# Performance work log

Measured on AMD Instinct MI355X. Metric: run time of the kernel, lower is better.

The kernel has to match this reference:

```python
import jax, jax.numpy as jnp
import numpy as np

N_NODES = 100000
N_EDGES = 1600000
HIDDEN = 128
STEPS = 4
N_GRAPHS = 64


def setup_inputs() -> dict:
    key = jax.random.key(0)
    ks = jax.random.split(key, 8)
    x = jax.random.normal(ks[0], (N_NODES, HIDDEN), dtype=jnp.float32)
    edge_index = jax.random.randint(ks[1], (2, N_EDGES), 0, N_NODES, dtype=jnp.int64)
    batch = jnp.sort(jax.random.randint(ks[2], (N_NODES,), 0, N_GRAPHS, dtype=jnp.int64))
    s = 1.0 / np.sqrt(HIDDEN)
    weight = jax.random.normal(ks[3], (STEPS, HIDDEN, HIDDEN), dtype=jnp.float32) * s
    w_ih = jax.random.normal(ks[4], (3 * HIDDEN, HIDDEN), dtype=jnp.float32) * s
    w_hh = jax.random.normal(ks[5], (3 * HIDDEN, HIDDEN), dtype=jnp.float32) * s
    b_ih = jnp.zeros((3 * HIDDEN,), dtype=jnp.float32)
    b_hh = jnp.zeros((3 * HIDDEN,), dtype=jnp.float32)
    return {"x": x, "edge_index": edge_index, "batch": batch,
            "weight": weight, "w_ih": w_ih, "w_hh": w_hh,
            "b_ih": b_ih, "b_hh": b_hh}


def _gru_cell(m, h, w_ih, w_hh, b_ih, b_hh):
    # PyTorch GRUCell: gates ordered (r, z, n)
    gi = m @ w_ih.T + b_ih  # [N, 3H]
    gh = h @ w_hh.T + b_hh  # [N, 3H]
    i_r, i_z, i_n = jnp.split(gi, 3, axis=-1)
    h_r, h_z, h_n = jnp.split(gh, 3, axis=-1)
    r = jax.nn.sigmoid(i_r + h_r)
    z = jax.nn.sigmoid(i_z + h_z)
    n = jnp.tanh(i_n + r * h_n)
    return (1.0 - z) * n + z * h


def reference(x, edge_index, batch, weight, w_ih, w_hh, b_ih, b_hh):
    src, dst = edge_index[0], edge_index[1]
    h = x
    for i in range(STEPS):
        m = h @ weight[i]  # [N, H]
        # message = m[src] scattered (add) into dst
        aggr = jax.ops.segment_sum(m[src], dst, num_segments=N_NODES)
        h = _gru_cell(aggr, h, w_ih, w_hh, b_ih, b_hh)
    h = jax.nn.relu(h)
    # global mean pool per graph
    sums = jax.ops.segment_sum(h, batch, num_segments=N_GRAPHS)  # [G, H]
    counts = jax.ops.segment_sum(jnp.ones((N_NODES,), h.dtype), batch, num_segments=N_GRAPHS)
    return sums / jnp.maximum(counts, 1.0)[:, None]
```

## Files before the change

### kernel.cpp

```cpp
#include <hip/hip_runtime.h>

#define N_NODES  100000
#define N_EDGES  1600000
#define HIDDEN   128
#define STEPS    4
#define N_GRAPHS 64
#define NBUCK    256
#define BWID     391
#define BCAP     7168

typedef unsigned short u16;
typedef unsigned int   u32;
typedef unsigned long long u64;
typedef __attribute__((ext_vector_type(8))) short bf16x8;
typedef __attribute__((ext_vector_type(4))) float f32x4;
typedef __attribute__((ext_vector_type(2))) float f32x2;

__device__ inline u16 f2bf(float f) {
  u32 u = __float_as_uint(f);
  u = (u + 0x7FFFu + ((u >> 16) & 1u)) >> 16;
  return (u16)u;
}
__device__ inline float bf2f(u16 b) { return __uint_as_float(((u32)b) << 16); }

__device__ inline float rcp_f(float x) { return __builtin_amdgcn_rcpf(x); }
__device__ inline float sig_f(float x) { return rcp_f(1.f + __expf(-x)); }
__device__ inline float tanh_f(float x) { return 1.f - 2.f * rcp_f(1.f + __expf(2.f * x)); }

__global__ __launch_bounds__(1024) void k_part(const int* __restrict__ esrc,
                                               const int* __restrict__ edst,
                                               int* __restrict__ gcursor,
                                               u32* __restrict__ ebuf) {
  __shared__ int hist[16][NBUCK];
  __shared__ int base[16][NBUCK];
  int tid = threadIdx.x;
  int wv  = tid >> 6;
  #pragma unroll
  for (int i = 0; i < 4; ++i) ((int*)hist)[tid + i * 1024] = 0;
  __syncthreads();
  int e0 = blockIdx.x * 4096;
  int sv[4], dv[4], bk[4], rk[4];
  #pragma unroll
  for (int i = 0; i < 4; ++i) {
    int e = e0 + i * 1024 + tid;
    if (e < N_EDGES) {
      sv[i] = esrc[e];
      dv[i] = edst[e];
      bk[i] = (int)((u32)dv[i] / (u32)BWID);
      rk[i] = atomicAdd(&hist[wv][bk[i]], 1);
    } else bk[i] = -1;
  }
  __syncthreads();
  if (tid < NBUCK) {
    int c[16];
    int sum = 0;
    #pragma unroll
    for (int w = 0; w < 16; ++w) { c[w] = hist[w][tid]; sum += c[w]; }
    int g = atomicAdd(&gcursor[tid], sum);
    #pragma unroll
    for (int w = 0; w < 16; ++w) { base[w][tid] = g; g += c[w]; }
  }
  __syncthreads();
  #pragma unroll
  for (int i = 0; i < 4; ++i) {
    if (bk[i] >= 0) {
      int pos = bk[i] * BCAP + base[wv][bk[i]] + rk[i];
      ebuf[pos] = ((u32)(dv[i] - bk[i] * BWID) << 17) | (u32)sv[i];
    }
  }
}

__global__ void k_bscan(const int* __restrict__ gcursor, int* __restrict__ ebase,
                        float* __restrict__ acc) {
  __shared__ int buf[NBUCK];
  int t = threadIdx.x;
  int v = gcursor[t];
  buf[t] = v;
  __syncthreads();
  for (int off = 1; off < NBUCK; off <<= 1) {
    int u = 0;
    if (t >= off) u = buf[t - off];
    __syncthreads();
    buf[t] += u;
    __syncthreads();
  }
  ebase[t] = buf[t] - v;
  if (t == NBUCK - 1) ebase[NBUCK] = buf[t];
  for (int i = t; i < N_GRAPHS * HIDDEN; i += NBUCK) acc[i] = 0.f;
}

__global__ __launch_bounds__(1024) void k_csr(const u32* __restrict__ ebuf,
                                              const int* __restrict__ ebase,
                                              int* __restrict__ offs,
                                              int* __restrict__ csr) {
  __shared__ int lcnt[512];
  __shared__ int lofs[512];
  int b = blockIdx.x, tid = threadIdx.x;
  int n0 = b * BWID;
  int n1 = min(n0 + BWID, N_NODES);
  int nn = n1 - n0;
  int e0 = ebase[b];
  int cnt = ebase[b + 1] - e0;
  const u32* ebase_p = ebuf + (size_t)b * BCAP;
  if (tid < 512) lcnt[tid] = 0;
  __syncthreads();
  for (int e = tid; e < cnt; e += 1024) {
    int dst = (int)(ebase_p[e] >> 17);
    atomicAdd(&lcnt[dst], 1);
  }
  __syncthreads();
  if (tid < 512) lofs[tid] = lcnt[tid];
  __syncthreads();
  for (int off = 1; off < 512; off <<= 1) {
    int v = 0;
    if (tid < 512 && tid >= off) v = lofs[tid - off];
    __syncthreads();
    if (tid < 512 && tid >= off) lofs[tid] += v;
    __syncthreads();
  }
  int nodeoff = 0;
  if (tid < 512) nodeoff = e0 + lofs[tid] - lcnt[tid];
  if (tid < 512) lofs[tid] = nodeoff;
  if (tid < nn) offs[n0 + tid] = nodeoff;
  if (b == 0 && tid == 0) offs[N_NODES] = N_EDGES;
  __syncthreads();
  for (int e = tid; e < cnt; e += 1024) {
    u32 p = ebase_p[e];
    int src = (int)(p & 0x1FFFFu);
    int dst = (int)(p >> 17);
    int pos = atomicAdd(&lofs[dst], 1);
    csr[pos] = src;
  }
}

__global__ void k_wb(const float* __restrict__ W, const float* __restrict__ w_ih,
                     const float* __restrict__ w_hh, u16* __restrict__ bsw) {
  __shared__ float wrow[128];
  int b = blockIdx.x, st = b >> 8, k = b & 255, t = threadIdx.x;
  if (k < 128) wrow[t] = W[(st * 128 + k) * 128 + t];
  __syncthreads();
  int kc = k >> 5, quad = (k >> 3) & 3, kl = k & 7;
  u16* base = bsw + (size_t)st * 131072 + kc * 16384;
  #pragma unroll
  for (int gq = 0; gq < 4; ++gq) {
    int c = gq * 128 + t;
    float v;
    if (k < 128) {
      if (c < 384) {
        const float* wr = w_ih + c * 128;
        float sacc = 0.f;
        for (int j = 0; j < 128; ++j) sacc += wrow[j] * wr[j];
        v = sacc;
      } else v = 0.f;
    } else {
      int kk = k - 128;
      if (c < 256)      v = w_hh[c * 128 + kk];
      else if (c < 384) v = 0.f;
      else              v = w_hh[(c - 128) * 128 + kk];
    }
    int gi = c >> 7, cw = c & 127;
    int wv = cw >> 5, hu = (cw >> 4) & 1, nl = c & 15;
    int slot = wv * 8 + gi * 2 + hu;
    base[(slot * 4 + quad) * 128 + nl * 8 + kl] = f2bf(v);
  }
}

__global__ void k_convert(const float* __restrict__ x, u16* __restrict__ h0,
                          u16* __restrict__ h1) {
  int i = (blockIdx.x * 256 + threadIdx.x) * 4;
  float4 v = *(const float4*)(x + i);
  u16 o[4] = {f2bf(v.x), f2bf(v.y), f2bf(v.z), f2bf(v.w)};
  *(uint2*)(h0 + i) = *(uint2*)o;
  if (blockIdx.x == 0) {
    int t = threadIdx.x;
    if (t < 64)       ((u32*)(h0 + (size_t)N_NODES * 128))[t] = 0;
    else if (t < 128) ((u32*)(h1 + (size_t)N_NODES * 128))[t - 64] = 0;
  }
}

__device__ inline void acc8(f32x2* a, uint4 p) {
  f32x2 v;
  v.x = __uint_as_float(p.x << 16); v.y = __uint_as_float(p.x & 0xffff0000u);
  a[0] += v;
  v.x = __uint_as_float(p.y << 16); v.y = __uint_as_float(p.y & 0xffff0000u);
  a[1] += v;
  v.x = __uint_as_float(p.z << 16); v.y = __uint_as_float(p.z & 0xffff0000u);
  a[2] += v;
  v.x = __uint_as_float(p.w << 16); v.y = __uint_as_float(p.w & 0xffff0000u);
  a[3] += v;
}
__device__ inline uint4 ldrow(const char* hb, u32 off) {
  return *(const uint4*)(hb + off);
}

__global__ void k_gather(const u16* __restrict__ h, const int* __restrict__ csr,
                         const int* __restrict__ offs, u16* __restrict__ s) {
  int node = blockIdx.x * 4 + (threadIdx.x >> 6);
  int lane = threadIdx.x & 63;
  int q   = lane >> 4;
  int sub = lane & 15;
  const char* hb = (const char*)h;
  u32 co = (u32)(sub * 16);
  int beg = offs[node], end = offs[node + 1];
  f32x2 a[4];
  a[0] = a[1] = a[2] = a[3] = (f32x2){0.f, 0.f};
  int j = beg + q;
  for (; j + 12 < end; j += 16) {
    u32 s0 = (u32)csr[j], s1 = (u32)csr[j + 4], s2 = (u32)csr[j + 8], s3 = (u32)csr[j + 12];
    uint4 p0 = ldrow(hb, (s0 << 8) | co);
    uint4 p1 = ldrow(hb, (s1 << 8) | co);
    uint4 p2 = ldrow(hb, (s2 << 8) | co);
    uint4 p3 = ldrow(hb, (s3 << 8) | co);
    acc8(a, p0); acc8(a, p1); acc8(a, p2); acc8(a, p3);
  }
  {
    int j0 = j, j1 = j + 4, j2 = j + 8, j3 = j + 12;
    int t0 = (j0 < end) ? j0 : 0, t1 = (j1 < end) ? j1 : 0;
    int t2 = (j2 < end) ? j2 : 0, t3 = (j3 < end) ? j3 : 0;
    u32 s0 = (u32)csr[t0]; s0 = (j0 < end) ? s0 : (u32)N_NODES;
    u32 s1 = (u32)csr[t1]; s1 = (j1 < end) ? s1 : (u32)N_NODES;
    u32 s2 = (u32)csr[t2]; s2 = (j2 < end) ? s2 : (u32)N_NODES;
    u32 s3 = (u32)csr[t3]; s3 = (j3 < end) ? s3 : (u32)N_NODES;
    uint4 p0 = ldrow(hb, (s0 << 8) | co);
    uint4 p1 = ldrow(hb, (s1 << 8) | co);
    uint4 p2 = ldrow(hb, (s2 << 8) | co);
    uint4 p3 = ldrow(hb, (s3 << 8) | co);
    acc8(a, p0); acc8(a, p1); acc8(a, p2); acc8(a, p3);
  }
  #pragma unroll
  for (int i = 0; i < 4; ++i) {
    a[i].x += __shfl_xor(a[i].x, 16); a[i].x += __shfl_xor(a[i].x, 32);
    a[i].y += __shfl_xor(a[i].y, 16); a[i].y += __shfl_xor(a[i].y, 32);
  }
  if (q == 0) {
    uint4 o;
    o.x = (u32)f2bf(a[0].x) | ((u32)f2bf(a[0].y) << 16);
    o.y = (u32)f2bf(a[1].x) | ((u32)f2bf(a[1].y) << 16);
    o.z = (u32)f2bf(a[2].x) | ((u32)f2bf(a[2].y) << 16);
    o.w = (u32)f2bf(a[3].x) | ((u32)f2bf(a[3].y) << 16);
    *(uint4*)(s + (size_t)node * 128 + sub * 8) = o;
  }
}

__global__ __launch_bounds__(256, 2) void k_gemm_gru(
    const u16* __restrict__ s_mat, const u16* __restrict__ h_mat,
    const u16* __restrict__ bsw, const float* __restrict__ b_ih,
    const float* __restrict__ b_hh, u16* __restrict__ h_out) {
  __shared__ u16 Asw[8192];

  const int tid  = threadIdx.x;
  const int wave = tid >> 6;
  const int lane = tid & 63;
  const int nl   = lane & 15;
  const int quad = lane >> 4;
  const int row0 = blockIdx.x * 32;

  {
    int snl = tid & 15, squad = (tid >> 4) & 3, sel = tid >> 6;
    int g = sel & 1, half = sel >> 1;
    const u16* row = (half ? h_mat : s_mat) + (size_t)(row0 + g * 16 + snl) * 128;
    #pragma unroll
    for (int kc2 = 0; kc2 < 4; ++kc2) {
      uint4 v = *(const uint4*)(row + kc2 * 32 + squad * 8);
      *(uint4*)&Asw[(((g * 8 + half * 4 + kc2) * 4 + squad) * 16 + snl) * 8] = v;
    }
  }
  __syncthreads();

  const u16* bp = bsw + wave * 8 * 512 + lane * 8;

  f32x4 acc[2][8];
  #pragma unroll
  for (int g = 0; g < 2; ++g)
    #pragma unroll
    for (int u = 0; u < 8; ++u) acc[g][u] = (f32x4){0.f, 0.f, 0.f, 0.f};

  bf16x8 b0[6], b1[6], b2[6];
  #pragma unroll
  for (int i = 0; i < 6; ++i) b0[i] = *(const bf16x8*)(bp + i * 512);
  #pragma unroll
  for (int i = 0; i < 6; ++i) b1[i] = *(const bf16x8*)(bp + 16384 + i * 512);

  #pragma unroll
  for (int kc = 0; kc < 8; ++kc) {
    if (kc < 6) {
      #pragma unroll
      for (int i = 0; i < 6; ++i) {
        int us = (kc + 2 < 4) ? i : (i < 4 ? i : i + 2);
        b2[i] = *(const bf16x8*)(bp + (kc + 2) * 16384 + us * 512);
      }
    }
    bf16x8 a0 = *(const bf16x8*)&Asw[kc * 512 + lane * 8];
    bf16x8 a1 = *(const bf16x8*)&Asw[(8 + kc) * 512 + lane * 8];
    #pragma unroll
    for (int i = 0; i < 6; ++i) {
      int u = (kc < 4) ? i : (i < 4 ? i : i + 2);
      acc[0][u] = __builtin_amdgcn_mfma_f32_16x16x32_bf16(a0, b0[i], acc[0][u], 0, 0, 0);
      acc[1][u] = __builtin_amdgcn_mfma_f32_16x16x32_bf16(a1, b0[i], acc[1][u], 0, 0, 0);
    }
    #pragma unroll
    for (int i = 0; i < 6; ++i) { b0[i] = b1[i]; b1[i] = b2[i]; }
  }

  float bias[8];
  #pragma unroll
  for (int u = 0; u < 8; ++u) {
    int gi = u >> 1, hu = u & 1;
    int cw = wave * 32 + hu * 16 + nl;
    bias[u] = (gi == 0) ? b_ih[cw] + b_hh[cw]
            : (gi == 1) ? b_ih[128 + cw] + b_hh[128 + cw]
            : (gi == 2) ? b_ih[256 + cw]
                        : b_hh[256 + cw];
  }

  #pragma unroll
  for (int g = 0; g < 2; ++g) {
    #pragma unroll
    for (int hu = 0; hu < 2; ++hu) {
      int cw = wave * 32 + hu * 16 + nl;
      int hbase = ((g * 8 + 4 + wave) * 4 + ((hu * 2 + (nl >> 3)) & 3)) * 128 + (nl & 7);
      #pragma unroll
      for (int i = 0; i < 4; ++i) {
        int m = quad * 4 + i;
        float rv = sig_f(acc[g][0 + hu][i] + bias[0 + hu]);
        float zv = sig_f(acc[g][2 + hu][i] + bias[2 + hu]);
        float iv = acc[g][4 + hu][i] + bias[4 + hu];
        float hn = acc[g][6 + hu][i] + bias[6 + hu];
        float hv = bf2f(Asw[hbase + m * 8]);
        float n  = tanh_f(iv + rv * hn);
        float o  = n + zv * (hv - n);
        h_out[(size_t)(row0 + g * 16 + m) * 128 + cw] = f2bf(o);
      }
    }
  }
}

__global__ void k_pool_partial(const u16* __restrict__ h, const int* __restrict__ batch,
                               float* __restrict__ acc) {
  int t = threadIdx.x;
  int node0 = blockIdx.x * 125;
  int node1 = node0 + 125;
  int cur = batch[node0];
  float sum = 0.f;
  for (int r = node0; r < node1; ++r) {
    int g = batch[r];
    if (g != cur) {
      atomicAdd(&acc[cur * 128 + t], sum);
      sum = 0.f;
      cur = g;
    }
    sum += fmaxf(bf2f(h[(size_t)r * 128 + t]), 0.f);
  }
  atomicAdd(&acc[cur * 128 + t], sum);
}

__global__ void k_pool_div(const float* __restrict__ acc, const int* __restrict__ batch,
                           float* __restrict__ out) {
  __shared__ int se[2];
  int g = blockIdx.x, t = threadIdx.x;
  if (t < 2) {
    int target = g + t;
    int lo = 0, hi = N_NODES;
    while (lo < hi) { int mid = (lo + hi) >> 1; if (batch[mid] < target) lo = mid + 1; else hi = mid; }
    se[t] = lo;
  }
  __syncthreads();
  int cnt = se[1] - se[0];
  out[g * 128 + t] = acc[g * 128 + t] / (float)(cnt > 0 ? cnt : 1);
}

extern "C" void kernel_launch(void* const* d_in, const int* in_sizes, int n_in,
                              void* d_out, int out_size, void* d_ws, size_t ws_size,
                              hipStream_t stream) {
  const float* x     = (const float*)d_in[0];
  const int*   edges = (const int*)d_in[1];
  const int*   batch = (const int*)d_in[2];
  const float* W     = (const float*)d_in[3];
  const float* w_ih  = (const float*)d_in[4];
  const float* w_hh  = (const float*)d_in[5];
  const float* b_ih  = (const float*)d_in[6];
  const float* b_hh  = (const float*)d_in[7];
  float* out = (float*)d_out;

  char* w = (char*)d_ws;
  u16* buf0    = (u16*)(w);
  u16* buf1    = (u16*)(w + 25600256);
  u16* bsw     = (u16*)(w + 51200512);
  float* acc   = (float*)(w + 52249088);
  int* offs    = (int*)(w + 52281856);
  int* gcursor = (int*)(w + 52682240);
  int* ebase   = (int*)(w + 52683264);
  int* csr     = (int*)(w + 52684800);
  u32* ebuf    = (u32*)buf1;

  const int* esrc = edges;
  const int* edst = edges + N_EDGES;

  hipMemsetAsync(gcursor, 0, NBUCK * sizeof(int), stream);
  k_part<<<391, 1024, 0, stream>>>(esrc, edst, gcursor, ebuf);
  k_bscan<<<1, NBUCK, 0, stream>>>(gcursor, ebase, acc);
  k_csr<<<NBUCK, 1024, 0, stream>>>(ebuf, ebase, offs, csr);
  k_wb<<<1024, 128, 0, stream>>>(W, w_ih, w_hh, bsw);
  k_convert<<<(N_NODES * HIDDEN) / 1024, 256, 0, stream>>>(x, buf0, buf1);

  u16* hcur = buf0;
  u16* hnxt = buf1;
  for (int st = 0; st < STEPS; ++st) {
    k_gather<<<N_NODES / 4, 256, 0, stream>>>(hcur, csr, offs, hnxt);
    k_gemm_gru<<<N_NODES / 32, 256, 0, stream>>>(hnxt, hcur, bsw + st * 131072,
                                                 b_ih, b_hh, hnxt);
    u16* tmp = hcur; hcur = hnxt; hnxt = tmp;
  }
  k_pool_partial<<<800, 128, 0, stream>>>(hcur, batch, acc);
  k_pool_div<<<N_GRAPHS, 128, 0, stream>>>(acc, batch, out);
}
```

Baseline: 585.5 us.

## Fuse neighbor gather into GEMM+GRU kernel, staging aggregates in shared memory

Merges the per-step CSR gather kernel into the GEMM+GRU kernel. Each wave gathers 8 nodes' neighbor sums and writes them as bf16 directly into the swizzled shared-memory A tile, while the h half is still loaded from global. This removes the global write and re-read of the aggregated matrix and one launch per step. The cost is that the latency-bound gather now runs at the GEMM's low occupancy (launch bounds of 256 threads, 2 blocks), with each wave walking its 8 nodes in sequence, so load latency may be poorly hidden.

New measurement: 616.7 us. 1.05x slower.

```diff
diff --git a/kernel.cpp b/kernel.cpp
--- a/kernel.cpp
+++ b/kernel.cpp
@@ -193,59 +193,11 @@
   return *(const uint4*)(hb + off);
 }
 
-__global__ void k_gather(const u16* __restrict__ h, const int* __restrict__ csr,
-                         const int* __restrict__ offs, u16* __restrict__ s) {
-  int node = blockIdx.x * 4 + (threadIdx.x >> 6);
-  int lane = threadIdx.x & 63;
-  int q   = lane >> 4;
-  int sub = lane & 15;
-  const char* hb = (const char*)h;
-  u32 co = (u32)(sub * 16);
-  int beg = offs[node], end = offs[node + 1];
-  f32x2 a[4];
-  a[0] = a[1] = a[2] = a[3] = (f32x2){0.f, 0.f};
-  int j = beg + q;
-  for (; j + 12 < end; j += 16) {
-    u32 s0 = (u32)csr[j], s1 = (u32)csr[j + 4], s2 = (u32)csr[j + 8], s3 = (u32)csr[j + 12];
-    uint4 p0 = ldrow(hb, (s0 << 8) | co);
-    uint4 p1 = ldrow(hb, (s1 << 8) | co);
-    uint4 p2 = ldrow(hb, (s2 << 8) | co);
-    uint4 p3 = ldrow(hb, (s3 << 8) | co);
-    acc8(a, p0); acc8(a, p1); acc8(a, p2); acc8(a, p3);
-  }
-  {
-    int j0 = j, j1 = j + 4, j2 = j + 8, j3 = j + 12;
-    int t0 = (j0 < end) ? j0 : 0, t1 = (j1 < end) ? j1 : 0;
-    int t2 = (j2 < end) ? j2 : 0, t3 = (j3 < end) ? j3 : 0;
-    u32 s0 = (u32)csr[t0]; s0 = (j0 < end) ? s0 : (u32)N_NODES;
-    u32 s1 = (u32)csr[t1]; s1 = (j1 < end) ? s1 : (u32)N_NODES;
-    u32 s2 = (u32)csr[t2]; s2 = (j2 < end) ? s2 : (u32)N_NODES;
-    u32 s3 = (u32)csr[t3]; s3 = (j3 < end) ? s3 : (u32)N_NODES;
-    uint4 p0 = ldrow(hb, (s0 << 8) | co);
-    uint4 p1 = ldrow(hb, (s1 << 8) | co);
-    uint4 p2 = ldrow(hb, (s2 << 8) | co);
-    uint4 p3 = ldrow(hb, (s3 << 8) | co);
-    acc8(a, p0); acc8(a, p1); acc8(a, p2); acc8(a, p3);
-  }
-  #pragma unroll
-  for (int i = 0; i < 4; ++i) {
-    a[i].x += __shfl_xor(a[i].x, 16); a[i].x += __shfl_xor(a[i].x, 32);
-    a[i].y += __shfl_xor(a[i].y, 16); a[i].y += __shfl_xor(a[i].y, 32);
-  }
-  if (q == 0) {
-    uint4 o;
-    o.x = (u32)f2bf(a[0].x) | ((u32)f2bf(a[0].y) << 16);
-    o.y = (u32)f2bf(a[1].x) | ((u32)f2bf(a[1].y) << 16);
-    o.z = (u32)f2bf(a[2].x) | ((u32)f2bf(a[2].y) << 16);
-    o.w = (u32)f2bf(a[3].x) | ((u32)f2bf(a[3].y) << 16);
-    *(uint4*)(s + (size_t)node * 128 + sub * 8) = o;
-  }
-}
-
-__global__ __launch_bounds__(256, 2) void k_gemm_gru(
-    const u16* __restrict__ s_mat, const u16* __restrict__ h_mat,
-    const u16* __restrict__ bsw, const float* __restrict__ b_ih,
-    const float* __restrict__ b_hh, u16* __restrict__ h_out) {
+__global__ __launch_bounds__(256, 2) void k_fused(
+    const u16* __restrict__ h_mat, const int* __restrict__ csr,
+    const int* __restrict__ offs, const u16* __restrict__ bsw,
+    const float* __restrict__ b_ih, const float* __restrict__ b_hh,
+    u16* __restrict__ h_out) {
   __shared__ u16 Asw[8192];
 
   const int tid  = threadIdx.x;
@@ -257,12 +209,66 @@
 
   {
     int snl = tid & 15, squad = (tid >> 4) & 3, sel = tid >> 6;
-    int g = sel & 1, half = sel >> 1;
-    const u16* row = (half ? h_mat : s_mat) + (size_t)(row0 + g * 16 + snl) * 128;
-    #pragma unroll
-    for (int kc2 = 0; kc2 < 4; ++kc2) {
-      uint4 v = *(const uint4*)(row + kc2 * 32 + squad * 8);
-      *(uint4*)&Asw[(((g * 8 + half * 4 + kc2) * 4 + squad) * 16 + snl) * 8] = v;
+    if (sel >= 2) {
+      int g = sel & 1;
+      const u16* row = h_mat + (size_t)(row0 + g * 16 + snl) * 128;
+      #pragma unroll
+      for (int kc2 = 0; kc2 < 4; ++kc2) {
+        uint4 v = *(const uint4*)(row + kc2 * 32 + squad * 8);
+        *(uint4*)&Asw[(((g * 8 + 4 + kc2) * 4 + squad) * 16 + snl) * 8] = v;
+      }
+    }
+  }
+
+  {
+    const char* hb = (const char*)h_mat;
+    const int q   = lane >> 4;
+    const int sub = lane & 15;
+    const u32 co  = (u32)(sub * 16);
+    #pragma unroll 1
+    for (int i = 0; i < 8; ++i) {
+      int n    = wave * 8 + i;
+      int node = row0 + n;
+      int beg = offs[node], end = offs[node + 1];
+      f32x2 a[4];
+      a[0] = a[1] = a[2] = a[3] = (f32x2){0.f, 0.f};
+      int j = beg + q;
+      for (; j + 12 < end; j += 16) {
+        u32 s0 = (u32)csr[j], s1 = (u32)csr[j + 4], s2 = (u32)csr[j + 8], s3 = (u32)csr[j + 12];
+        uint4 p0 = ldrow(hb, (s0 << 8) | co);
+        uint4 p1 = ldrow(hb, (s1 << 8) | co);
+        uint4 p2 = ldrow(hb, (s2 << 8) | co);
+        uint4 p3 = ldrow(hb, (s3 << 8) | co);
+        acc8(a, p0); acc8(a, p1); acc8(a, p2); acc8(a, p3);
+      }
+      {
+        int j0 = j, j1 = j + 4, j2 = j + 8, j3 = j + 12;
+        int t0 = (j0 < end) ? j0 : 0, t1 = (j1 < end) ? j1 : 0;
+        int t2 = (j2 < end) ? j2 : 0, t3 = (j3 < end) ? j3 : 0;
+        u32 s0 = (u32)csr[t0]; s0 = (j0 < end) ? s0 : (u32)N_NODES;
+        u32 s1 = (u32)csr[t1]; s1 = (j1 < end) ? s1 : (u32)N_NODES;
+        u32 s2 = (u32)csr[t2]; s2 = (j2 < end) ? s2 : (u32)N_NODES;
+        u32 s3 = (u32)csr[t3]; s3 = (j3 < end) ? s3 : (u32)N_NODES;
+        uint4 p0 = ldrow(hb, (s0 << 8) | co);
+        uint4 p1 = ldrow(hb, (s1 << 8) | co);
+        uint4 p2 = ldrow(hb, (s2 << 8) | co);
+        uint4 p3 = ldrow(hb, (s3 << 8) | co);
+        acc8(a, p0); acc8(a, p1); acc8(a, p2); acc8(a, p3);
+      }
+      #pragma unroll
+      for (int r = 0; r < 4; ++r) {
+        a[r].x += __shfl_xor(a[r].x, 16); a[r].x += __shfl_xor(a[r].x, 32);
+        a[r].y += __shfl_xor(a[r].y, 16); a[r].y += __shfl_xor(a[r].y, 32);
+      }
+      if (q == 0) {
+        uint4 o;
+        o.x = (u32)f2bf(a[0].x) | ((u32)f2bf(a[0].y) << 16);
+        o.y = (u32)f2bf(a[1].x) | ((u32)f2bf(a[1].y) << 16);
+        o.z = (u32)f2bf(a[2].x) | ((u32)f2bf(a[2].y) << 16);
+        o.w = (u32)f2bf(a[3].x) | ((u32)f2bf(a[3].y) << 16);
+        int g = n >> 4, snl = n & 15;
+        *(uint4*)&Asw[(((g * 8 + (sub >> 2)) * 4 + (sub & 3)) * 16 + snl) * 8] = o;
+      }
     }
   }
   __syncthreads();
@@ -406,9 +412,8 @@
   u16* hcur = buf0;
   u16* hnxt = buf1;
   for (int st = 0; st < STEPS; ++st) {
-    k_gather<<<N_NODES / 4, 256, 0, stream>>>(hcur, csr, offs, hnxt);
-    k_gemm_gru<<<N_NODES / 32, 256, 0, stream>>>(hnxt, hcur, bsw + st * 131072,
-                                                 b_ih, b_hh, hnxt);
+    k_fused<<<N_NODES / 32, 256, 0, stream>>>(hcur, csr, offs, bsw + st * 131072,
+                                              b_ih, b_hh, hnxt);
     u16* tmp = hcur; hcur = hnxt; hnxt = tmp;
   }
   k_pool_partial<<<800, 128, 0, stream>>>(hcur, batch, acc);
```

## Store node features in column slabs and gather per slab

Applied to the files above, without the earlier changes.

Node features are now stored as 8 column slabs of 16 bf16 values each, instead of row-major 128-wide rows. The neighbour-aggregation kernel is rewritten so that each block handles 32 nodes for one slab. The GEMM/GRU, pooling and conversion kernels are adapted to the new layout. The intent is to shrink the working set each gather touches so it stays in cache. The cost is 32-byte random row accesses instead of 256-byte ones, which may waste cache-line bandwidth, and uses more blocks. Separately, the input conversion is fused into the weight-preparation kernel to save a launch.

New measurement: 619.4 us. 5.8% more time.

```diff
diff --git a/kernel.cpp b/kernel.cpp
--- a/kernel.cpp
+++ b/kernel.cpp
@@ -8,6 +8,8 @@
 #define NBUCK    256
 #define BWID     391
 #define BCAP     7168
+#define SLABU    1600016
+#define SLABB    3200032
 
 typedef unsigned short u16;
 typedef unsigned int   u32;
@@ -133,10 +135,31 @@
   }
 }
 
-__global__ void k_wb(const float* __restrict__ W, const float* __restrict__ w_ih,
-                     const float* __restrict__ w_hh, u16* __restrict__ bsw) {
+__global__ void k_wbc(const float* __restrict__ W, const float* __restrict__ w_ih,
+                      const float* __restrict__ w_hh, u16* __restrict__ bsw,
+                      const float* __restrict__ x, u16* __restrict__ h0,
+                      u16* __restrict__ h1) {
   __shared__ float wrow[128];
+  if (blockIdx.x >= 1024) {
+    int bb = blockIdx.x - 1024;
+    int i = (bb * 256 + threadIdx.x) * 4;
+    float4 v = *(const float4*)(x + i);
+    u16 o[4] = {f2bf(v.x), f2bf(v.y), f2bf(v.z), f2bf(v.w)};
+    int row = i >> 7, col = i & 127;
+    *(uint2*)(h0 + (size_t)(col >> 4) * SLABU + (size_t)row * 16 + (col & 15)) = *(uint2*)o;
+    if (bb == 0) {
+      int t = threadIdx.x;
+      if (t < 64) {
+        ((u32*)h0)[(size_t)(t >> 3) * (SLABU / 2) + (N_NODES * 8) + (t & 7)] = 0;
+      } else if (t < 128) {
+        int tt = t - 64;
+        ((u32*)h1)[(size_t)(tt >> 3) * (SLABU / 2) + (N_NODES * 8) + (tt & 7)] = 0;
+      }
+    }
+    return;
+  }
   int b = blockIdx.x, st = b >> 8, k = b & 255, t = threadIdx.x;
+  if (t >= 128) return;
   if (k < 128) wrow[t] = W[(st * 128 + k) * 128 + t];
   __syncthreads();
   int kc = k >> 5, quad = (k >> 3) & 3, kl = k & 7;
@@ -165,19 +188,6 @@
   }
 }
 
-__global__ void k_convert(const float* __restrict__ x, u16* __restrict__ h0,
-                          u16* __restrict__ h1) {
-  int i = (blockIdx.x * 256 + threadIdx.x) * 4;
-  float4 v = *(const float4*)(x + i);
-  u16 o[4] = {f2bf(v.x), f2bf(v.y), f2bf(v.z), f2bf(v.w)};
-  *(uint2*)(h0 + i) = *(uint2*)o;
-  if (blockIdx.x == 0) {
-    int t = threadIdx.x;
-    if (t < 64)       ((u32*)(h0 + (size_t)N_NODES * 128))[t] = 0;
-    else if (t < 128) ((u32*)(h1 + (size_t)N_NODES * 128))[t - 64] = 0;
-  }
-}
-
 __device__ inline void acc8(f32x2* a, uint4 p) {
   f32x2 v;
   v.x = __uint_as_float(p.x << 16); v.y = __uint_as_float(p.x & 0xffff0000u);
@@ -193,52 +203,57 @@
   return *(const uint4*)(hb + off);
 }
 
-__global__ void k_gather(const u16* __restrict__ h, const int* __restrict__ csr,
-                         const int* __restrict__ offs, u16* __restrict__ s) {
-  int node = blockIdx.x * 4 + (threadIdx.x >> 6);
-  int lane = threadIdx.x & 63;
-  int q   = lane >> 4;
-  int sub = lane & 15;
-  const char* hb = (const char*)h;
-  u32 co = (u32)(sub * 16);
-  int beg = offs[node], end = offs[node + 1];
+__global__ void k_gather_sliced(const u16* __restrict__ h, const int* __restrict__ csr,
+                                const int* __restrict__ offs, u16* __restrict__ s) {
+  __shared__ int soffs[33];
+  const int tid   = threadIdx.x;
+  const int slice = blockIdx.x & 7;
+  const int tile  = blockIdx.x >> 3;
+  const int row0  = tile * 32;
+  if (tid < 33) soffs[tid] = offs[row0 + tid];
+  __syncthreads();
+  const int wave = tid >> 6;
+  const int lane = tid & 63;
+  const int no   = lane >> 3;
+  const int slot = (lane >> 1) & 3;
+  const int hf   = lane & 1;
+  const int n    = wave * 8 + no;
+  const char* hb = (const char*)h + (size_t)slice * SLABB;
+  const u32 co   = (u32)(hf << 4);
+  int beg = soffs[n], end = soffs[n + 1];
+  int dm = end - beg;
+  dm = max(dm, __shfl_xor(dm, 8));
+  dm = max(dm, __shfl_xor(dm, 16));
+  dm = max(dm, __shfl_xor(dm, 32));
+  int iters = (dm + 7) >> 3;
   f32x2 a[4];
   a[0] = a[1] = a[2] = a[3] = (f32x2){0.f, 0.f};
-  int j = beg + q;
-  for (; j + 12 < end; j += 16) {
-    u32 s0 = (u32)csr[j], s1 = (u32)csr[j + 4], s2 = (u32)csr[j + 8], s3 = (u32)csr[j + 12];
-    uint4 p0 = ldrow(hb, (s0 << 8) | co);
-    uint4 p1 = ldrow(hb, (s1 << 8) | co);
-    uint4 p2 = ldrow(hb, (s2 << 8) | co);
-    uint4 p3 = ldrow(hb, (s3 << 8) | co);
-    acc8(a, p0); acc8(a, p1); acc8(a, p2); acc8(a, p3);
-  }
-  {
-    int j0 = j, j1 = j + 4, j2 = j + 8, j3 = j + 12;
-    int t0 = (j0 < end) ? j0 : 0, t1 = (j1 < end) ? j1 : 0;
-    int t2 = (j2 < end) ? j2 : 0, t3 = (j3 < end) ? j3 : 0;
-    u32 s0 = (u32)csr[t0]; s0 = (j0 < end) ? s0 : (u32)N_NODES;
-    u32 s1 = (u32)csr[t1]; s1 = (j1 < end) ? s1 : (u32)N_NODES;
-    u32 s2 = (u32)csr[t2]; s2 = (j2 < end) ? s2 : (u32)N_NODES;
-    u32 s3 = (u32)csr[t3]; s3 = (j3 < end) ? s3 : (u32)N_NODES;
-    uint4 p0 = ldrow(hb, (s0 << 8) | co);
-    uint4 p1 = ldrow(hb, (s1 << 8) | co);
-    uint4 p2 = ldrow(hb, (s2 << 8) | co);
-    uint4 p3 = ldrow(hb, (s3 << 8) | co);
-    acc8(a, p0); acc8(a, p1); acc8(a, p2); acc8(a, p3);
-  }
-  #pragma unroll
-  for (int i = 0; i < 4; ++i) {
-    a[i].x += __shfl_xor(a[i].x, 16); a[i].x += __shfl_xor(a[i].x, 32);
-    a[i].y += __shfl_xor(a[i].y, 16); a[i].y += __shfl_xor(a[i].y, 32);
-  }
-  if (q == 0) {
+  int j0 = beg + slot;
+  #pragma unroll 1
+  for (int t = 0; t < iters; ++t) {
+    int ja = j0 + t * 8;
+    int jb = ja + 4;
+    u32 sa = (u32)csr[ja < end ? ja : 0];
+    u32 sb = (u32)csr[jb < end ? jb : 0];
+    sa = (ja < end) ? sa : (u32)N_NODES;
+    sb = (jb < end) ? sb : (u32)N_NODES;
+    uint4 ra = ldrow(hb, (sa << 5) | co);
+    uint4 rb = ldrow(hb, (sb << 5) | co);
+    acc8(a, ra);
+    acc8(a, rb);
+  }
+  #pragma unroll
+  for (int r = 0; r < 4; ++r) {
+    a[r].x += __shfl_xor(a[r].x, 2); a[r].y += __shfl_xor(a[r].y, 2);
+    a[r].x += __shfl_xor(a[r].x, 4); a[r].y += __shfl_xor(a[r].y, 4);
+  }
+  if ((lane & 6) == 0) {
     uint4 o;
     o.x = (u32)f2bf(a[0].x) | ((u32)f2bf(a[0].y) << 16);
     o.y = (u32)f2bf(a[1].x) | ((u32)f2bf(a[1].y) << 16);
     o.z = (u32)f2bf(a[2].x) | ((u32)f2bf(a[2].y) << 16);
     o.w = (u32)f2bf(a[3].x) | ((u32)f2bf(a[3].y) << 16);
-    *(uint4*)(s + (size_t)node * 128 + sub * 8) = o;
+    *(uint4*)(s + (size_t)slice * SLABU + (size_t)(row0 + n) * 16 + hf * 8) = o;
   }
 }
 
@@ -258,10 +273,12 @@
   {
     int snl = tid & 15, squad = (tid >> 4) & 3, sel = tid >> 6;
     int g = sel & 1, half = sel >> 1;
-    const u16* row = (half ? h_mat : s_mat) + (size_t)(row0 + g * 16 + snl) * 128;
+    const u16* mat = half ? h_mat : s_mat;
+    size_t r = (size_t)(row0 + g * 16 + snl);
     #pragma unroll
     for (int kc2 = 0; kc2 < 4; ++kc2) {
-      uint4 v = *(const uint4*)(row + kc2 * 32 + squad * 8);
+      int slab = kc2 * 2 + (squad >> 1);
+      uint4 v = *(const uint4*)(mat + (size_t)slab * SLABU + r * 16 + (squad & 1) * 8);
       *(uint4*)&Asw[(((g * 8 + half * 4 + kc2) * 4 + squad) * 16 + snl) * 8] = v;
     }
   }
@@ -318,6 +335,7 @@
     #pragma unroll
     for (int hu = 0; hu < 2; ++hu) {
       int cw = wave * 32 + hu * 16 + nl;
+      int slab = wave * 2 + hu;
       int hbase = ((g * 8 + 4 + wave) * 4 + ((hu * 2 + (nl >> 3)) & 3)) * 128 + (nl & 7);
       #pragma unroll
       for (int i = 0; i < 4; ++i) {
@@ -329,7 +347,7 @@
         float hv = bf2f(Asw[hbase + m * 8]);
         float n  = tanh_f(iv + rv * hn);
         float o  = n + zv * (hv - n);
-        h_out[(size_t)(row0 + g * 16 + m) * 128 + cw] = f2bf(o);
+        h_out[(size_t)slab * SLABU + (size_t)(row0 + g * 16 + m) * 16 + nl] = f2bf(o);
       }
     }
   }
@@ -338,8 +356,9 @@
 __global__ void k_pool_partial(const u16* __restrict__ h, const int* __restrict__ batch,
                                float* __restrict__ acc) {
   int t = threadIdx.x;
-  int node0 = blockIdx.x * 125;
-  int node1 = node0 + 125;
+  size_t cbase = (size_t)(t >> 4) * SLABU + (t & 15);
+  int node0 = blockIdx.x * 80;
+  int node1 = node0 + 80;
   int cur = batch[node0];
   float sum = 0.f;
   for (int r = node0; r < node1; ++r) {
@@ -349,7 +368,7 @@
       sum = 0.f;
       cur = g;
     }
-    sum += fmaxf(bf2f(h[(size_t)r * 128 + t]), 0.f);
+    sum += fmaxf(bf2f(h[cbase + (size_t)r * 16]), 0.f);
   }
   atomicAdd(&acc[cur * 128 + t], sum);
 }
@@ -400,17 +419,17 @@
   k_part<<<391, 1024, 0, stream>>>(esrc, edst, gcursor, ebuf);
   k_bscan<<<1, NBUCK, 0, stream>>>(gcursor, ebase, acc);
   k_csr<<<NBUCK, 1024, 0, stream>>>(ebuf, ebase, offs, csr);
-  k_wb<<<1024, 128, 0, stream>>>(W, w_ih, w_hh, bsw);
-  k_convert<<<(N_NODES * HIDDEN) / 1024, 256, 0, stream>>>(x, buf0, buf1);
+  k_wbc<<<1024 + (N_NODES * HIDDEN) / 1024, 256, 0, stream>>>(W, w_ih, w_hh, bsw,
+                                                              x, buf0, buf1);
 
   u16* hcur = buf0;
   u16* hnxt = buf1;
   for (int st = 0; st < STEPS; ++st) {
-    k_gather<<<N_NODES / 4, 256, 0, stream>>>(hcur, csr, offs, hnxt);
+    k_gather_sliced<<<(N_NODES / 32) * 8, 256, 0, stream>>>(hcur, csr, offs, hnxt);
     k_gemm_gru<<<N_NODES / 32, 256, 0, stream>>>(hnxt, hcur, bsw + st * 131072,
                                                  b_ih, b_hh, hnxt);
     u16* tmp = hcur; hcur = hnxt; hnxt = tmp;
   }
-  k_pool_partial<<<800, 128, 0, stream>>>(hcur, batch, acc);
+  k_pool_partial<<<1250, 128, 0, stream>>>(hcur, batch, acc);
   k_pool_div<<<N_GRAPHS, 128, 0, stream>>>(acc, batch, out);
 }
```
